# Performance work log

Measured on AMD Instinct MI355X. Metric: run time of the kernel, lower is better.

The kernel has to match this reference:

```python
import jax, jax.numpy as jnp
import numpy as np

N = 16384   # num_nodes (also in_channels: identity-style features)
C = 256     # hidden channels
K = 16      # num_classes
E = 524288  # num edges


def gcn_conv(x, src, dst, ew, W, b, num_nodes):
    """PyG GCNConv: linear transform, then sym-normalized scatter-add aggregation.
    Self-loops (weight 1) are appended; norm = d^-1/2[src] * w * d^-1/2[dst]."""
    h = x @ W                                            # [N, out]
    loop = jnp.arange(num_nodes, dtype=src.dtype)
    s = jnp.concatenate([src, loop])
    d = jnp.concatenate([dst, loop])
    w = jnp.concatenate([ew, jnp.ones((num_nodes,), ew.dtype)])
    deg = jax.ops.segment_sum(w, d, num_segments=num_nodes)
    dinv = jnp.where(deg > 0, jax.lax.rsqrt(jnp.maximum(deg, 1e-12)), 0.0)
    norm = dinv[s] * w * dinv[d]                         # [E+N]
    msg = norm[:, None] * h[s]                           # gather + scale
    out = jax.ops.segment_sum(msg, d, num_segments=num_nodes)  # scatter-add
    return out + b


def setup_inputs() -> dict:
    key = jax.random.key(0)
    k1, k2, k3, k4, k5, k6, k7 = jax.random.split(key, 7)
    x = jax.random.normal(k1, (N, N), dtype=jnp.float32)
    edge_index = jax.random.randint(k2, (2, E), 0, N, dtype=jnp.int64)
    edge_weight = jax.random.uniform(k3, (E,), dtype=jnp.float32)
    # GCNConv parameters (glorot-ish scale)
    W1 = jax.random.normal(k4, (N, C), dtype=jnp.float32) / np.sqrt(N)
    b1 = jnp.zeros((C,), jnp.float32)
    W2 = jax.random.normal(k5, (C, K), dtype=jnp.float32) / np.sqrt(C)
    b2 = jnp.zeros((K,), jnp.float32)
    return {"x": x, "edge_index": edge_index, "edge_weight": edge_weight,
            "W1": W1, "b1": b1, "W2": W2, "b2": b2}


def reference(x, edge_index, edge_weight, W1, b1, W2, b2):
    src, dst = edge_index[0], edge_index[1]
    h = gcn_conv(x, src, dst, edge_weight, W1, b1, N)
    h = jax.nn.relu(h)
    # dropout p=0.5 is identity in eval mode (self.training == False)
    out = gcn_conv(h, src, dst, edge_weight, W2, b2, N)
    return out
```

## Files before the change

kernel.cpp:

```cpp
#include <hip/hip_runtime.h>
#include <stdint.h>


namespace {
constexpr int NN = 16384;
constexpr int CH = 256;
constexpr int KC = 16;
constexpr int NE = 524288;
constexpr int KD = 16384;
constexpr int KSPLIT = 4;
constexpr int BM = 128;

constexpr size_t OFF_W1T  = 0;
constexpr size_t OFF_HP   = 8388608;
constexpr size_t OFF_HB   = 75497472;
constexpr size_t OFF_OUT1 = 83886080;
constexpr size_t OFF_H2   = 100663296;
constexpr size_t OFF_DEG  = 101711872;
constexpr size_t OFF_CNT  = 101777408;
constexpr size_t OFF_DINV = 101842944;
constexpr size_t OFF_ROWP = 101908480;
constexpr size_t OFF_CUR  = 102039552;
constexpr size_t OFF_COLS = 102105088;
constexpr size_t OFF_NRM  = 104202240;
}

typedef __attribute__((ext_vector_type(8))) short bf16x8;
typedef __attribute__((ext_vector_type(4))) float f32x4;

__device__ __forceinline__ unsigned short f2bf(float f) {
  unsigned int u = __builtin_bit_cast(unsigned int, f);
  u += 0x7fffu + ((u >> 16) & 1u);
  return (unsigned short)(u >> 16);
}
__device__ __forceinline__ float bf2f(unsigned short v) {
  unsigned int u = ((unsigned int)v) << 16;
  return __builtin_bit_cast(float, u);
}

__global__ __launch_bounds__(256)
void k_w1t(const float* __restrict__ w1, unsigned short* __restrict__ w1t) {
  __shared__ float tile[64][65];
  const int t = threadIdx.x;
  const int kb = blockIdx.x * 64;
  const int nb = blockIdx.y * 64;
  const int r = t >> 6;
  const int c = t & 63;
#pragma unroll
  for (int i = 0; i < 16; ++i)
    tile[i * 4 + r][c] = w1[(size_t)(kb + i * 4 + r) * CH + nb + c];
  __syncthreads();
#pragma unroll
  for (int i = 0; i < 16; ++i)
    w1t[(size_t)(nb + i * 4 + r) * KD + kb + c] = f2bf(tile[c][i * 4 + r]);
}

__global__ __launch_bounds__(256)
void k_deg(const int* __restrict__ dst, const float* __restrict__ ew,
           float* __restrict__ deg, int* __restrict__ cnt) {
  const int e = blockIdx.x * 256 + threadIdx.x;
  const int d = dst[e];
  atomicAdd(&deg[d], ew[e]);
  atomicAdd(&cnt[d], 1);
}

__global__ __launch_bounds__(256)
void k_dinv(const float* __restrict__ deg, float* __restrict__ dinv) {
  const int i = blockIdx.x * 256 + threadIdx.x;
  dinv[i] = rsqrtf(deg[i] + 1.0f);
}

__global__ __launch_bounds__(256)
void k_scan(const int* __restrict__ cnt, int* __restrict__ rowp, int* __restrict__ curs) {
  __shared__ int ps[256];
  const int t = threadIdx.x;
  const int base = t * 64;
  int s = 0;
  for (int j = 0; j < 64; ++j) s += cnt[base + j];
  ps[t] = s;
  __syncthreads();
  int v = s;
  for (int off = 1; off < 256; off <<= 1) {
    int u = (t >= off) ? ps[t - off] : 0;
    __syncthreads();
    v += u;
    ps[t] = v;
    __syncthreads();
  }
  int run = v - s;
  for (int j = 0; j < 64; ++j) {
    int c = cnt[base + j];
    rowp[base + j] = run;
    curs[base + j] = run;
    run += c;
  }
  if (t == 255) rowp[NN] = run;
}

__global__ __launch_bounds__(256)
void k_fill(const int* __restrict__ src, const int* __restrict__ dst,
            const float* __restrict__ ew, const float* __restrict__ dinv,
            int* __restrict__ curs, int* __restrict__ cols, float* __restrict__ nrm) {
  const int e = blockIdx.x * 256 + threadIdx.x;
  const int s = src[e], d = dst[e];
  const int pos = atomicAdd(&curs[d], 1);
  cols[pos] = s;
  nrm[pos] = dinv[s] * ew[e] * dinv[d];
}

__global__ __launch_bounds__(256)
void k_gemm1(const float* __restrict__ x, const unsigned short* __restrict__ w1t,
             float* __restrict__ hp) {
  __shared__ __align__(16) unsigned short As[2][BM * 32];
  __shared__ __align__(16) unsigned short Bs[2][256 * 32];

  const int tid  = threadIdx.x;
  const int lane = tid & 63;
  const int wave = tid >> 6;

  const int bid  = blockIdx.x;
  const int xcd  = bid & 7;
  const int slot = bid >> 3;
  const int kb   = xcd >> 1;
  const int bm0  = (slot * 2 + (xcd & 1)) * BM;
  const int koff = kb * (KD / KSPLIT);
  const int wn0  = wave * 64;

  const int r0  = tid >> 2;
  const int kq  = tid & 3;
  const int acn = kq ^ ((r0 >> 1) & 3);
  const int aoff0 = r0 * 32 + acn * 8;
  const int aoff1 = (r0 + 64) * 32 + acn * 8;

  const int cc = (lane & 3) ^ ((lane >> 3) & 3);
  const unsigned short* bbase =
      w1t + (size_t)(wave * 64 + (lane >> 2)) * KD + koff + cc * 8;

  const int fr = lane & 15, fg = lane >> 4;
  const int fch = fg ^ ((fr >> 1) & 3);
  const int fA = fr * 32 + fch * 8;
  const int fB = (wn0 + fr) * 32 + fch * 8;

  const float* xrow0 = x + (size_t)(bm0 + r0) * KD + koff + kq * 8;
  const float* xrow1 = xrow0 + (size_t)64 * KD;

  float4 a00, a01, a10, a11;
  f32x4 acc[8][4] = {};

  auto GLOADB = [&](int t, int buf) {
    const unsigned short* g = bbase + (size_t)t * 32;
#pragma unroll
    for (int i = 0; i < 4; ++i) {
      __builtin_amdgcn_global_load_lds(
          (const __attribute__((address_space(1))) void*)(g + (size_t)i * 16 * KD),
          (__attribute__((address_space(3))) void*)(&Bs[buf][(wave * 64 + i * 16) * 32]),
          16, 0, 0);
    }
  };
  auto LOADA = [&](int t) {
    const float* p0 = xrow0 + (size_t)t * 32;
    const float* p1 = xrow1 + (size_t)t * 32;
    a00 = *reinterpret_cast<const float4*>(p0);
    a01 = *reinterpret_cast<const float4*>(p0 + 4);
    a10 = *reinterpret_cast<const float4*>(p1);
    a11 = *reinterpret_cast<const float4*>(p1 + 4);
  };
  auto STOREA = [&](int buf) {
    bf16x8 v;
    v[0] = (short)f2bf(a00.x); v[1] = (short)f2bf(a00.y);
    v[2] = (short)f2bf(a00.z); v[3] = (short)f2bf(a00.w);
    v[4] = (short)f2bf(a01.x); v[5] = (short)f2bf(a01.y);
    v[6] = (short)f2bf(a01.z); v[7] = (short)f2bf(a01.w);
    *reinterpret_cast<bf16x8*>(&As[buf][aoff0]) = v;
    v[0] = (short)f2bf(a10.x); v[1] = (short)f2bf(a10.y);
    v[2] = (short)f2bf(a10.z); v[3] = (short)f2bf(a10.w);
    v[4] = (short)f2bf(a11.x); v[5] = (short)f2bf(a11.y);
    v[6] = (short)f2bf(a11.z); v[7] = (short)f2bf(a11.w);
    *reinterpret_cast<bf16x8*>(&As[buf][aoff1]) = v;
  };

  constexpr int NT = KD / KSPLIT / 32;
  GLOADB(0, 0);
  LOADA(0);
  STOREA(0);
  __syncthreads();
  int cur = 0;

  for (int t = 0; t < NT; ++t) {
    if (t + 1 < NT) {
      GLOADB(t + 1, cur ^ 1);
      LOADA(t + 1);
    }
    bf16x8 bfr[4];
#pragma unroll
    for (int ni = 0; ni < 4; ++ni)
      bfr[ni] = *reinterpret_cast<const bf16x8*>(&Bs[cur][fB + ni * 512]);
#pragma unroll
    for (int mi = 0; mi < 8; ++mi) {
      const bf16x8 af = *reinterpret_cast<const bf16x8*>(&As[cur][fA + mi * 512]);
#pragma unroll
      for (int ni = 0; ni < 4; ++ni)
        acc[mi][ni] = __builtin_amdgcn_mfma_f32_16x16x32_bf16(af, bfr[ni], acc[mi][ni], 0, 0, 0);
    }
    if (t + 1 < NT) {
      STOREA(cur ^ 1);
      __syncthreads();
      cur ^= 1;
    }
  }

  float* hpo = hp + (size_t)kb * NN * CH;
#pragma unroll
  for (int mi = 0; mi < 8; ++mi)
#pragma unroll
    for (int ni = 0; ni < 4; ++ni)
#pragma unroll
      for (int r = 0; r < 4; ++r) {
        const int m = bm0 + mi * 16 + fg * 4 + r;
        const int n = wn0 + ni * 16 + fr;
        hpo[(size_t)m * CH + n] = acc[mi][ni][r];
      }
}

__global__ __launch_bounds__(256)
void k_hred(const float* __restrict__ hp, unsigned short* __restrict__ hb) {
  const size_t i = ((size_t)blockIdx.x * 256 + threadIdx.x) * 8;
  float s[8];
#pragma unroll
  for (int j = 0; j < 8; ++j) s[j] = 0.f;
#pragma unroll
  for (int p = 0; p < KSPLIT; ++p) {
    const float* q = hp + (size_t)p * NN * CH + i;
    const float4 v0 = *reinterpret_cast<const float4*>(q);
    const float4 v1 = *reinterpret_cast<const float4*>(q + 4);
    s[0] += v0.x; s[1] += v0.y; s[2] += v0.z; s[3] += v0.w;
    s[4] += v1.x; s[5] += v1.y; s[6] += v1.z; s[7] += v1.w;
  }
  bf16x8 o;
#pragma unroll
  for (int j = 0; j < 8; ++j) o[j] = (short)f2bf(s[j]);
  *reinterpret_cast<bf16x8*>(hb + i) = o;
}

__global__ __launch_bounds__(256)
void k_agg1(const unsigned short* __restrict__ hb, const int* __restrict__ rowp,
            const int* __restrict__ cols, const float* __restrict__ nrm,
            const float* __restrict__ dinv, const float* __restrict__ b1,
            float* __restrict__ out1) {
  __shared__ int   scols[64];
  __shared__ float snrm[64];
  const int i = blockIdx.x;
  const int c = threadIdx.x;
  const int beg = rowp[i], end = rowp[i + 1];
  const float di = dinv[i];
  float acc = di * di * bf2f(hb[(size_t)i * CH + c]);
  for (int base = beg; base < end; base += 64) {
    const int m = min(64, end - base);
    __syncthreads();
    if (c < m) { scols[c] = cols[base + c]; snrm[c] = nrm[base + c]; }
    __syncthreads();
    for (int j = 0; j < m; ++j)
      acc += snrm[j] * bf2f(hb[(size_t)scols[j] * CH + c]);
  }
  out1[(size_t)i * CH + c] = fmaxf(acc + b1[c], 0.0f);
}

__global__ __launch_bounds__(256)
void k_gemm2(const float* __restrict__ out1, const float* __restrict__ w2,
             float* __restrict__ h2) {
  __shared__ float xs[16][256];
  __shared__ float ws[256 * 16];
  const int t = threadIdx.x;
  const int n0 = blockIdx.x * 16;
#pragma unroll
  for (int i = 0; i < 16; ++i) ws[i * 256 + t] = w2[i * 256 + t];
#pragma unroll
  for (int i = 0; i < 16; ++i) xs[i][t] = out1[(size_t)(n0 + i) * CH + t];
  __syncthreads();
  const int node = t >> 4, k = t & 15;
  float acc = 0.f;
#pragma unroll 8
  for (int c = 0; c < 256; ++c) acc += xs[node][c] * ws[c * 16 + k];
  h2[(size_t)(n0 + node) * KC + k] = acc;
}

__global__ __launch_bounds__(256)
void k_agg2(const float* __restrict__ h2, const int* __restrict__ rowp,
            const int* __restrict__ cols, const float* __restrict__ nrm,
            const float* __restrict__ dinv, const float* __restrict__ b2,
            float* __restrict__ out) {
  const int i = blockIdx.x * 4 + (threadIdx.x >> 6);
  const int lane = threadIdx.x & 63;
  const int k = lane & 15, g = lane >> 4;
  const int beg = rowp[i], end = rowp[i + 1];
  float acc = 0.f;
  for (int e = beg + g; e < end; e += 4)
    acc += nrm[e] * h2[(size_t)cols[e] * KC + k];
  acc += __shfl_xor(acc, 16);
  acc += __shfl_xor(acc, 32);
  if (g == 0) {
    const float di = dinv[i];
    out[(size_t)i * KC + k] = acc + di * di * h2[(size_t)i * KC + k] + b2[k];
  }
}

extern "C" void kernel_launch(void* const* d_in, const int* in_sizes, int n_in,
                              void* d_out, int out_size, void* d_ws, size_t ws_size,
                              hipStream_t stream) {
  const float* x  = (const float*)d_in[0];
  const int*   ei = (const int*)d_in[1];
  const float* ew = (const float*)d_in[2];
  const float* w1 = (const float*)d_in[3];
  const float* b1 = (const float*)d_in[4];
  const float* w2 = (const float*)d_in[5];
  const float* b2 = (const float*)d_in[6];
  const int* src = ei;
  const int* dst = ei + NE;

  uint8_t* ws = (uint8_t*)d_ws;
  unsigned short* w1t = (unsigned short*)(ws + OFF_W1T);
  float* hp   = (float*)(ws + OFF_HP);
  unsigned short* hb = (unsigned short*)(ws + OFF_HB);
  float* out1 = (float*)(ws + OFF_OUT1);
  float* h2   = (float*)(ws + OFF_H2);
  float* deg  = (float*)(ws + OFF_DEG);
  int*   cnt  = (int*)(ws + OFF_CNT);
  float* dinv = (float*)(ws + OFF_DINV);
  int*   rowp = (int*)(ws + OFF_ROWP);
  int*   curs = (int*)(ws + OFF_CUR);
  int*   cols = (int*)(ws + OFF_COLS);
  float* nrm  = (float*)(ws + OFF_NRM);
  float* out  = (float*)d_out;

  hipMemsetAsync(ws + OFF_DEG, 0, 131072, stream);

  k_w1t <<<dim3(256, 4), 256, 0, stream>>>(w1, w1t);
  k_deg <<<NE / 256, 256, 0, stream>>>(dst, ew, deg, cnt);
  k_dinv<<<NN / 256, 256, 0, stream>>>(deg, dinv);
  k_scan<<<1, 256, 0, stream>>>(cnt, rowp, curs);
  k_fill<<<NE / 256, 256, 0, stream>>>(src, dst, ew, dinv, curs, cols, nrm);
  k_gemm1<<<(NN / BM) * KSPLIT, 256, 0, stream>>>(x, w1t, hp);
  k_hred<<<NN * CH / (256 * 8), 256, 0, stream>>>(hp, hb);
  k_agg1<<<NN, 256, 0, stream>>>(hb, rowp, cols, nrm, dinv, b1, out1);
  k_gemm2<<<NN / 16, 256, 0, stream>>>(out1, w2, h2);
  k_agg2<<<NN / 4, 256, 0, stream>>>(h2, rowp, cols, nrm, dinv, b2, out);
}
```

Baseline: 484.3 us.

## Split aggregation edges across waves and add MFMA priority in GEMM1

The layer-1 aggregation kernel now gives each wave a strided subset of a node's edges. Each lane loads four bf16 channels with a vector load, two edges are in flight per iteration, and the per-wave partial sums are reduced through shared memory. This replaces the old scheme, where all 256 threads walked every edge serially with 2-byte loads and two barriers per chunk of 64 edges. Separately, GEMM1 gets a launch-bounds occupancy hint of 2 blocks and raises wave priority around its MFMA loop. The occupancy hint may force register limits on a kernel holding large accumulator arrays.

```diff
diff --git a/kernel.cpp b/kernel.cpp
--- a/kernel.cpp
+++ b/kernel.cpp
@@ -108,7 +108,7 @@
   nrm[pos] = dinv[s] * ew[e] * dinv[d];
 }
 
-__global__ __launch_bounds__(256)
+__global__ __launch_bounds__(256, 2)
 void k_gemm1(const float* __restrict__ x, const unsigned short* __restrict__ w1t,
              float* __restrict__ hp) {
   __shared__ __align__(16) unsigned short As[2][BM * 32];
@@ -195,6 +195,7 @@
 #pragma unroll
     for (int ni = 0; ni < 4; ++ni)
       bfr[ni] = *reinterpret_cast<const bf16x8*>(&Bs[cur][fB + ni * 512]);
+    __builtin_amdgcn_s_setprio(1);
 #pragma unroll
     for (int mi = 0; mi < 8; ++mi) {
       const bf16x8 af = *reinterpret_cast<const bf16x8*>(&As[cur][fA + mi * 512]);
@@ -202,6 +203,7 @@
       for (int ni = 0; ni < 4; ++ni)
         acc[mi][ni] = __builtin_amdgcn_mfma_f32_16x16x32_bf16(af, bfr[ni], acc[mi][ni], 0, 0, 0);
     }
+    __builtin_amdgcn_s_setprio(0);
     if (t + 1 < NT) {
       STOREA(cur ^ 1);
       __syncthreads();
@@ -247,22 +249,36 @@
             const int* __restrict__ cols, const float* __restrict__ nrm,
             const float* __restrict__ dinv, const float* __restrict__ b1,
             float* __restrict__ out1) {
-  __shared__ int   scols[64];
-  __shared__ float snrm[64];
+  __shared__ float red[4][256];
   const int i = blockIdx.x;
-  const int c = threadIdx.x;
+  const int t = threadIdx.x;
+  const int w = t >> 6, l = t & 63;
   const int beg = rowp[i], end = rowp[i + 1];
+  float a0 = 0.f, a1 = 0.f, a2 = 0.f, a3 = 0.f;
+  int e = beg + w;
+  for (; e + 4 < end; e += 8) {
+    const int s0 = cols[e], s1 = cols[e + 4];
+    const float n0 = nrm[e], n1 = nrm[e + 4];
+    const ushort4 h0 = *reinterpret_cast<const ushort4*>(hb + (size_t)s0 * CH + l * 4);
+    const ushort4 h1 = *reinterpret_cast<const ushort4*>(hb + (size_t)s1 * CH + l * 4);
+    a0 += n0 * bf2f(h0.x) + n1 * bf2f(h1.x);
+    a1 += n0 * bf2f(h0.y) + n1 * bf2f(h1.y);
+    a2 += n0 * bf2f(h0.z) + n1 * bf2f(h1.z);
+    a3 += n0 * bf2f(h0.w) + n1 * bf2f(h1.w);
+  }
+  if (e < end) {
+    const int s0 = cols[e];
+    const float n0 = nrm[e];
+    const ushort4 h0 = *reinterpret_cast<const ushort4*>(hb + (size_t)s0 * CH + l * 4);
+    a0 += n0 * bf2f(h0.x); a1 += n0 * bf2f(h0.y);
+    a2 += n0 * bf2f(h0.z); a3 += n0 * bf2f(h0.w);
+  }
+  *reinterpret_cast<float4*>(&red[w][l * 4]) = make_float4(a0, a1, a2, a3);
+  __syncthreads();
   const float di = dinv[i];
-  float acc = di * di * bf2f(hb[(size_t)i * CH + c]);
-  for (int base = beg; base < end; base += 64) {
-    const int m = min(64, end - base);
-    __syncthreads();
-    if (c < m) { scols[c] = cols[base + c]; snrm[c] = nrm[base + c]; }
-    __syncthreads();
-    for (int j = 0; j < m; ++j)
-      acc += snrm[j] * bf2f(hb[(size_t)scols[j] * CH + c]);
-  }
-  out1[(size_t)i * CH + c] = fmaxf(acc + b1[c], 0.0f);
+  float sum = red[0][t] + red[1][t] + red[2][t] + red[3][t]
+            + di * di * bf2f(hb[(size_t)i * CH + t]) + b1[t];
+  out1[(size_t)i * CH + t] = fmaxf(sum, 0.0f);
 }
 
 __global__ __launch_bounds__(256)
```

Result: faster. 469.0 us (-3.1%).
